# Performance work log

Hardware: AMD Instinct MI355X
Metric: run time of the kernel (lower is better)

Reference implementation:

```python
import jax, jax.numpy as jnp
import numpy as np
import math

B, S, H, NH = 2, 2048, 2048, 16
HD = H // NH
BASE = 10000.0


def _rope_tables():
    inv_freq = 1.0 / (BASE ** (np.arange(0, HD, 2, dtype=np.float32) / HD))
    t = np.arange(S, dtype=np.float32)
    freqs = np.einsum('i,j->ij', t, inv_freq)          # [S, HD/2]
    emb = np.concatenate([freqs, freqs], axis=-1)       # [S, HD]
    return jnp.asarray(np.cos(emb)), jnp.asarray(np.sin(emb))


def setup_inputs() -> dict:
    key = jax.random.key(0)
    ks = jax.random.split(key, 6)
    scale = 1.0 / math.sqrt(H)
    cos, sin = _rope_tables()
    causal = np.triu(np.full((S, S), -1e9, dtype=np.float32), k=1)
    attn_bias = jnp.broadcast_to(jnp.asarray(causal)[None, None], (B, 1, S, S))
    return {
        'hidden_states': jax.random.normal(ks[0], (B, S, H), jnp.float32),
        'masks': jnp.zeros((B, S, S), jnp.float32),
        'attn_bias': attn_bias,
        'cos': cos,
        'sin': sin,
        'wq': jax.random.normal(ks[1], (H, H), jnp.float32) * scale,
        'wk': jax.random.normal(ks[2], (H, H), jnp.float32) * scale,
        'wv': jax.random.normal(ks[3], (H, H), jnp.float32) * scale,
        'wo': jax.random.normal(ks[4], (H, H), jnp.float32) * scale,
        'position_ids': jnp.broadcast_to(jnp.arange(S, dtype=jnp.int64)[None], (B, S)),
    }


def _rotate_half(x):
    x1, x2 = x[..., : x.shape[-1] // 2], x[..., x.shape[-1] // 2:]
    return jnp.concatenate([-x2, x1], axis=-1)


def reference(hidden_states, masks, attn_bias, cos, sin, wq, wk, wv, wo, position_ids):
    b, s, h = hidden_states.shape
    nh, hd = NH, HD
    # QKV projections (torch Linear: x @ W.T), split heads -> [b, nh, s, hd]
    def proj(w):
        return (hidden_states @ w.T).reshape(b, s, nh, hd).transpose(0, 2, 1, 3)
    q, k, v = proj(wq), proj(wk), proj(wv)
    # RoPE
    cos_p = cos[position_ids][:, None]  # [b, 1, s, hd]
    sin_p = sin[position_ids][:, None]
    q = q * cos_p + _rotate_half(q) * sin_p
    k = k * cos_p + _rotate_half(k) * sin_p
    # attention scores with additive masks (mx_attn branch, fp math)
    att = jnp.einsum('bhqd,bhkd->bhqk', q / math.sqrt(hd), k)
    att = att + attn_bias + masks[:, None]
    att = jax.nn.softmax(att, axis=-1)
    out = jnp.einsum('bhqk,bhkd->bhqd', att, v)
    out = out.transpose(0, 2, 1, 3).reshape(b, s, h)
    return out @ wo.T
```

## Files before the change

### kernel.cpp

```cpp
#include <hip/hip_runtime.h>
#include <stdint.h>

#define B_  2
#define S_  2048
#define H_  2048
#define NH_ 16
#define HD_ 128

typedef __bf16 v8bf __attribute__((ext_vector_type(8)));
typedef float  v4f  __attribute__((ext_vector_type(4)));

__device__ __forceinline__ float b2f(unsigned short u) {
  union { unsigned int i; float f; } x; x.i = ((unsigned int)u) << 16; return x.f;
}
__device__ __forceinline__ unsigned short f2b(float f) {
  union { float f; unsigned int i; } x; x.f = f;
  unsigned int r = x.i + 0x7FFFu + ((x.i >> 16) & 1u);
  return (unsigned short)(r >> 16);
}

__device__ __forceinline__ void async16(const void* g, void* l) {
  __builtin_amdgcn_global_load_lds(
      (const __attribute__((address_space(1))) void*)g,
      (__attribute__((address_space(3))) void*)l, 16, 0, 0);
}

__global__ __launch_bounds__(256) void cvt_all(const float* __restrict__ hid,
                                               const float* __restrict__ wq,
                                               const float* __restrict__ wk,
                                               const float* __restrict__ wv,
                                               const float* __restrict__ wo,
                                               unsigned short* __restrict__ Xb,
                                               unsigned short* __restrict__ Wqb,
                                               unsigned short* __restrict__ Wkb,
                                               unsigned short* __restrict__ Wvb,
                                               unsigned short* __restrict__ Wob) {
  int bid = blockIdx.x;
  const float* src;
  unsigned short* dst;
  int rel;
  if (bid < 8192)       { src = hid; dst = Xb;  rel = bid; }
  else if (bid < 12288) { src = wq;  dst = Wqb; rel = bid - 8192; }
  else if (bid < 16384) { src = wk;  dst = Wkb; rel = bid - 12288; }
  else if (bid < 20480) { src = wv;  dst = Wvb; rel = bid - 16384; }
  else                  { src = wo;  dst = Wob; rel = bid - 20480; }
  int i = rel * 256 + threadIdx.x;
  float4 f = *(const float4*)(src + (size_t)i * 4);
  ushort4 u;
  u.x = f2b(f.x); u.y = f2b(f.y); u.z = f2b(f.z); u.w = f2b(f.w);
  *(ushort4*)(dst + (size_t)i * 4) = u;
}

__device__ __forceinline__ void gemm_tile_nt(const unsigned short* __restrict__ A,
                                             const unsigned short* __restrict__ Bm,
                                             int m0, int n0, int Kdim,
                                             unsigned short* As, unsigned short* Bs,
                                             v4f (&acc)[2][8]) {
  const int tid = threadIdx.x;
  const int lane = tid & 63, w = tid >> 6;
  const int lr = lane & 15, lg = lane >> 4;
  const int wm = w * 32;

  for (int k0 = 0; k0 < Kdim; k0 += 32) {
    __syncthreads();
#pragma unroll
    for (int i = 0; i < 2; ++i) {
      const int cbase = i * 256 + w * 64;
      const int cc = cbase + lane;
      const int row = cc >> 2, col = (cc & 3) << 3;
      async16(A  + (size_t)(m0 + row) * Kdim + k0 + col, (char*)As + (size_t)cbase * 16);
      async16(Bm + (size_t)(n0 + row) * Kdim + k0 + col, (char*)Bs + (size_t)cbase * 16);
    }
    __syncthreads();
    v8bf a[2], bb[8];
#pragma unroll
    for (int i = 0; i < 2; i++) a[i]  = *(const v8bf*)(As + (wm + i * 16 + lr) * 32 + lg * 8);
#pragma unroll
    for (int i = 0; i < 8; i++) bb[i] = *(const v8bf*)(Bs + (i * 16 + lr) * 32 + lg * 8);
#pragma unroll
    for (int mi = 0; mi < 2; mi++)
#pragma unroll
      for (int ni = 0; ni < 8; ni++)
        acc[mi][ni] = __builtin_amdgcn_mfma_f32_16x16x32_bf16(a[mi], bb[ni], acc[mi][ni], 0, 0, 0);
  }
}

__global__ __launch_bounds__(512, 2) void gemm_qkv(const unsigned short* __restrict__ X,
                                                   const unsigned short* __restrict__ Wq,
                                                   const unsigned short* __restrict__ Wk,
                                                   const unsigned short* __restrict__ Wv,
                                                   const float* __restrict__ cosT,
                                                   const float* __restrict__ sinT,
                                                   unsigned short* __restrict__ Qo,
                                                   unsigned short* __restrict__ Ko,
                                                   unsigned short* __restrict__ Vt) {
  __shared__ __align__(16) unsigned short lds[4][256 * 64];

  const int tid = threadIdx.x, lane = tid & 63, w = tid >> 6;
  const int lr = lane & 15, lg = lane >> 4;
  const int wm = w >> 1, wn = w & 1;
  const int m0 = blockIdx.x * 256;
  const int ny = blockIdx.y;
  const int sel = ny >> 3;
  const int nt = ny & 7;
  const int n0 = nt * 256;
  const unsigned short* Bw = (sel == 0) ? Wq : (sel == 1 ? Wk : Wv);
  const int xsw = (lr & 7) << 3;

  auto stg = [&](const unsigned short* G, int g0, int k0, unsigned short* dst) {
#pragma unroll
    for (int i = 0; i < 4; ++i) {
      const int cbase = i * 512 + w * 64;
      const int cc = cbase + lane;
      const int row = cc >> 3;
      const int kq = (cc & 7) ^ (row & 7);
      async16(G + (size_t)(g0 + row) * H_ + k0 + kq * 8, (char*)dst + (size_t)cbase * 16);
    }
  };

  v4f acc[4][8];
#pragma unroll
  for (int i = 0; i < 4; i++)
#pragma unroll
    for (int j = 0; j < 8; j++) { v4f z = {0.f, 0.f, 0.f, 0.f}; acc[i][j] = z; }

  stg(X,  m0, 0, lds[0]);
  stg(Bw, n0, 0, lds[1]);
  __syncthreads();

  for (int t = 0; t < 32; ++t) {
    const unsigned short* As = lds[(t & 1) * 2];
    const unsigned short* Bs = lds[(t & 1) * 2 + 1];
    unsigned short* Ad = lds[((t + 1) & 1) * 2];
    unsigned short* Bd = lds[((t + 1) & 1) * 2 + 1];
    const int kn = (t + 1) * 64;
    v8bf bf[8][2], af[2];

    if (t < 31) stg(X, m0, kn, Ad);
#pragma unroll
    for (int ni = 0; ni < 8; ni++) {
      const unsigned short* rp = Bs + (size_t)(wn * 128 + ni * 16 + lr) * 64;
      bf[ni][0] = *(const v8bf*)(rp + ((lg * 8) ^ xsw));
      bf[ni][1] = *(const v8bf*)(rp + ((32 + lg * 8) ^ xsw));
    }
    {
      const unsigned short* rp = As + (size_t)(wm * 64 + lr) * 64;
      af[0] = *(const v8bf*)(rp + ((lg * 8) ^ xsw));
      af[1] = *(const v8bf*)(rp + ((32 + lg * 8) ^ xsw));
    }
    __builtin_amdgcn_s_barrier();
    asm volatile("s_waitcnt lgkmcnt(0)" ::: "memory");
    __builtin_amdgcn_sched_barrier(0);
    __builtin_amdgcn_s_setprio(1);
#pragma unroll
    for (int ni = 0; ni < 8; ni++) {
      acc[0][ni] = __builtin_amdgcn_mfma_f32_16x16x32_bf16(af[0], bf[ni][0], acc[0][ni], 0, 0, 0);
      acc[0][ni] = __builtin_amdgcn_mfma_f32_16x16x32_bf16(af[1], bf[ni][1], acc[0][ni], 0, 0, 0);
    }
    __builtin_amdgcn_s_setprio(0);
    __builtin_amdgcn_s_barrier();

    if (t < 31) stg(Bw, n0, kn, Bd);
    {
      const unsigned short* rp = As + (size_t)(wm * 64 + 16 + lr) * 64;
      af[0] = *(const v8bf*)(rp + ((lg * 8) ^ xsw));
      af[1] = *(const v8bf*)(rp + ((32 + lg * 8) ^ xsw));
    }
    __builtin_amdgcn_s_barrier();
    asm volatile("s_waitcnt lgkmcnt(0)" ::: "memory");
    __builtin_amdgcn_sched_barrier(0);
    __builtin_amdgcn_s_setprio(1);
#pragma unroll
    for (int ni = 0; ni < 8; ni++) {
      acc[1][ni] = __builtin_amdgcn_mfma_f32_16x16x32_bf16(af[0], bf[ni][0], acc[1][ni], 0, 0, 0);
      acc[1][ni] = __builtin_amdgcn_mfma_f32_16x16x32_bf16(af[1], bf[ni][1], acc[1][ni], 0, 0, 0);
    }
    __builtin_amdgcn_s_setprio(0);
    __builtin_amdgcn_s_barrier();

    {
      const unsigned short* rp = As + (size_t)(wm * 64 + 32 + lr) * 64;
      af[0] = *(const v8bf*)(rp + ((lg * 8) ^ xsw));
      af[1] = *(const v8bf*)(rp + ((32 + lg * 8) ^ xsw));
    }
    __builtin_amdgcn_s_barrier();
    asm volatile("s_waitcnt lgkmcnt(0)" ::: "memory");
    __builtin_amdgcn_sched_barrier(0);
    __builtin_amdgcn_s_setprio(1);
#pragma unroll
    for (int ni = 0; ni < 8; ni++) {
      acc[2][ni] = __builtin_amdgcn_mfma_f32_16x16x32_bf16(af[0], bf[ni][0], acc[2][ni], 0, 0, 0);
      acc[2][ni] = __builtin_amdgcn_mfma_f32_16x16x32_bf16(af[1], bf[ni][1], acc[2][ni], 0, 0, 0);
    }
    __builtin_amdgcn_s_setprio(0);
    __builtin_amdgcn_s_barrier();

    {
      const unsigned short* rp = As + (size_t)(wm * 64 + 48 + lr) * 64;
      af[0] = *(const v8bf*)(rp + ((lg * 8) ^ xsw));
      af[1] = *(const v8bf*)(rp + ((32 + lg * 8) ^ xsw));
    }
    __builtin_amdgcn_s_barrier();
    asm volatile("s_waitcnt lgkmcnt(0)" ::: "memory");
    __builtin_amdgcn_sched_barrier(0);
    __builtin_amdgcn_s_setprio(1);
#pragma unroll
    for (int ni = 0; ni < 8; ni++) {
      acc[3][ni] = __builtin_amdgcn_mfma_f32_16x16x32_bf16(af[0], bf[ni][0], acc[3][ni], 0, 0, 0);
      acc[3][ni] = __builtin_amdgcn_mfma_f32_16x16x32_bf16(af[1], bf[ni][1], acc[3][ni], 0, 0, 0);
    }
    __builtin_amdgcn_s_setprio(0);
    __syncthreads();
  }

  const int h = nt * 2 + wn;
  const int rb0 = m0 + wm * 64;
  if (sel < 2) {
    unsigned short* Out = (sel == 0) ? Qo : Ko;
    const float sc = (sel == 0) ? (float)(0.08838834764831845 * 1.4426950408889634) : 1.0f;
#pragma unroll
    for (int mi = 0; mi < 4; mi++)
#pragma unroll
      for (int ni = 0; ni < 4; ni++)
#pragma unroll
        for (int r = 0; r < 4; r++) {
          int row = rb0 + mi * 16 + lg * 4 + r;
          int s = row & 2047;
          int d = ni * 16 + lr;
          float c  = cosT[(size_t)s * HD_ + d];
          float sn = sinT[(size_t)s * HD_ + d];
          float x1 = acc[mi][ni][r], x2 = acc[mi][ni + 4][r];
          Out[(size_t)row * H_ + h * HD_ + d]      = f2b((x1 * c - x2 * sn) * sc);
          Out[(size_t)row * H_ + h * HD_ + d + 64] = f2b((x2 * c + x1 * sn) * sc);
        }
  } else {
#pragma unroll
    for (int mi = 0; mi < 4; mi++)
#pragma unroll
      for (int ni = 0; ni < 8; ni++) {
        int row0 = rb0 + mi * 16 + lg * 4;
        int b = row0 >> 11, s0 = row0 & 2047;
        int d = ni * 16 + lr;
        ushort4 u;
        u.x = f2b(acc[mi][ni][0]); u.y = f2b(acc[mi][ni][1]);
        u.z = f2b(acc[mi][ni][2]); u.w = f2b(acc[mi][ni][3]);
        *(ushort4*)(Vt + ((size_t)((b * NH_ + h) * HD_) + d) * S_ + s0) = u;
      }
  }
}

__global__ __launch_bounds__(256, 2) void gemm_out(const unsigned short* __restrict__ A,
                                                   const unsigned short* __restrict__ Wo,
                                                   float* __restrict__ Out) {
  __shared__ unsigned short As[128 * 32], Bs[128 * 32];
  const int m0 = blockIdx.x * 128;
  const int n0 = blockIdx.y * 128;

  v4f acc[2][8];
#pragma unroll
  for (int i = 0; i < 2; i++)
#pragma unroll
    for (int j = 0; j < 8; j++) { v4f z = {0.f, 0.f, 0.f, 0.f}; acc[i][j] = z; }

  gemm_tile_nt(A, Wo, m0, n0, H_, As, Bs, acc);

  const int lane = threadIdx.x & 63, w = threadIdx.x >> 6;
  const int lr = lane & 15, lg = lane >> 4;
#pragma unroll
  for (int mi = 0; mi < 2; mi++)
#pragma unroll
    for (int ni = 0; ni < 8; ni++)
#pragma unroll
      for (int r = 0; r < 4; r++)
        Out[(size_t)(m0 + w * 32 + mi * 16 + lg * 4 + r) * H_ + n0 + ni * 16 + lr] =
            acc[mi][ni][r];
}

#define KT_ 64

__global__ __launch_bounds__(512, 2) void attn_kernel(const unsigned short* __restrict__ Qb,
                                                      const unsigned short* __restrict__ Kb,
                                                      const unsigned short* __restrict__ Vt,
                                                      unsigned short* __restrict__ Ob) {
  __shared__ __align__(16) char smem[90112];
  unsigned short* Ps = (unsigned short*)(smem + 71680);

  const int tid = threadIdx.x, lane = tid & 63, w = tid >> 6;
  const int lr = lane & 15, lg = lane >> 4;
  const int qp = blockIdx.x, h = blockIdx.y, b = blockIdx.z;

  const int wtile = (w < 4) ? qp : (15 - qp);
  const int wrow = wtile * 128 + (w & 3) * 32;
  const int nkt = (16 - qp) * 2;

  auto stage = [&](int kt, char* Kd) {
    const int k0 = kt * KT_;
    char* Vd = Kd + 17408;
#pragma unroll
    for (int i = 0; i < 3; ++i) {
      int cbase = i * 512 + w * 64;
      if (cbase < 1088) {
        int cc = cbase + lane;
        int row = cc / 17, pos = cc % 17;
        int p2 = (pos == 16) ? 0 : pos;
        async16(Kb + (size_t)(b * S_ + k0 + row) * H_ + h * HD_ + p2 * 8,
                Kd + (size_t)cbase * 16);
      }
    }
#pragma unroll
    for (int i = 0; i < 3; ++i) {
      int cbase = i * 512 + w * 64;
      if (cbase < 1152) {
        int cc = cbase + lane;
        int row = cc / 9, pos = cc % 9;
        int p2 = (pos == 8) ? 0 : pos;
        async16(Vt + ((size_t)((b * NH_ + h) * HD_ + row)) * S_ + k0 + p2 * 8,
                Vd + (size_t)cbase * 16);
      }
    }
  };

  v8bf qf[2][4];
#pragma unroll
  for (int mt = 0; mt < 2; mt++)
#pragma unroll
    for (int ks = 0; ks < 4; ks++)
      qf[mt][ks] = *(const v8bf*)(Qb + (size_t)(b * S_ + wrow + mt * 16 + lr) * H_ +
                                  h * HD_ + ks * 32 + lg * 8);

  v4f o[2][8];
#pragma unroll
  for (int mt = 0; mt < 2; mt++)
#pragma unroll
    for (int nt = 0; nt < 8; nt++) { v4f z = {0.f, 0.f, 0.f, 0.f}; o[mt][nt] = z; }
  float mst[2][4], lst[2][4];
#pragma unroll
  for (int mt = 0; mt < 2; mt++)
#pragma unroll
    for (int r = 0; r < 4; r++) { mst[mt][r] = -1e30f; lst[mt][r] = 0.f; }

  stage(0, smem);
  __syncthreads();

  int cur = 0;
  for (int kt = 0; kt < nkt; kt++) {
    char* curb = smem + cur * 35840;
    if (kt + 1 < nkt) stage(kt + 1, smem + (cur ^ 1) * 35840);

    unsigned short* Ks = (unsigned short*)curb;
    unsigned short* Vs = (unsigned short*)(curb + 17408);
    const int k0 = kt * KT_;

    if (k0 <= wrow + 31) {
      v4f sacc[2][4];
#pragma unroll
      for (int mt = 0; mt < 2; mt++)
#pragma unroll
        for (int nt = 0; nt < 4; nt++) { v4f z = {0.f, 0.f, 0.f, 0.f}; sacc[mt][nt] = z; }
#pragma unroll
      for (int nt = 0; nt < 4; nt++) {
        v8bf kf[4];
#pragma unroll
        for (int ks = 0; ks < 4; ks++)
          kf[ks] = *(const v8bf*)(Ks + (nt * 16 + lr) * 136 + ks * 32 + lg * 8);
#pragma unroll
        for (int mt = 0; mt < 2; mt++)
#pragma unroll
          for (int ks = 0; ks < 4; ks++)
            sacc[mt][nt] =
                __builtin_amdgcn_mfma_f32_16x16x32_bf16(qf[mt][ks], kf[ks], sacc[mt][nt], 0, 0, 0);
      }
      if (k0 + KT_ - 1 > wrow) {
#pragma unroll
        for (int mt = 0; mt < 2; mt++)
#pragma unroll
          for (int nt = 0; nt < 4; nt++)
#pragma unroll
            for (int r = 0; r < 4; r++) {
              int key = k0 + nt * 16 + lr;
              int query = wrow + mt * 16 + lg * 4 + r;
              if (key > query) sacc[mt][nt][r] = -1e30f;
            }
      }
#pragma unroll
      for (int mt = 0; mt < 2; mt++) {
        float rmax[4], alpha[4], rsum[4];
#pragma unroll
        for (int r = 0; r < 4; r++) {
          float v = fmaxf(fmaxf(sacc[mt][0][r], sacc[mt][1][r]),
                          fmaxf(sacc[mt][2][r], sacc[mt][3][r]));
#pragma unroll
          for (int off = 8; off >= 1; off >>= 1) v = fmaxf(v, __shfl_xor(v, off, 64));
          rmax[r] = v;
        }
#pragma unroll
        for (int r = 0; r < 4; r++) {
          float mnew = fmaxf(mst[mt][r], rmax[r]);
          alpha[r] = exp2f(mst[mt][r] - mnew);
          mst[mt][r] = mnew;
          rsum[r] = 0.f;
        }
#pragma unroll
        for (int nt = 0; nt < 4; nt++)
#pragma unroll
          for (int r = 0; r < 4; r++) {
            float p = exp2f(sacc[mt][nt][r] - mst[mt][r]);
            sacc[mt][nt][r] = p;
            rsum[r] += p;
          }
#pragma unroll
        for (int r = 0; r < 4; r++) {
#pragma unroll
          for (int off = 8; off >= 1; off >>= 1) rsum[r] += __shfl_xor(rsum[r], off, 64);
          lst[mt][r] = lst[mt][r] * alpha[r] + rsum[r];
        }
#pragma unroll
        for (int nt = 0; nt < 8; nt++)
#pragma unroll
          for (int r = 0; r < 4; r++) o[mt][nt][r] *= alpha[r];
      }
      v8bf bv[8][2];
#pragma unroll
      for (int nt = 0; nt < 8; nt++)
#pragma unroll
        for (int ks = 0; ks < 2; ks++)
          bv[nt][ks] = *(const v8bf*)(Vs + (nt * 16 + lr) * 72 + ks * 32 + lg * 8);
#pragma unroll
      for (int mt = 0; mt < 2; mt++) {
#pragma unroll
        for (int nt = 0; nt < 4; nt++)
#pragma unroll
          for (int r = 0; r < 4; r++) {
            union { float f; unsigned u; } pu; pu.f = sacc[mt][nt][r];
            Ps[w * 1152 + (lg * 4 + r) * 72 + nt * 16 + lr] =
                (unsigned short)(pu.u >> 16);
          }
        asm volatile("" ::: "memory");
        v8bf af[2];
#pragma unroll
        for (int ks = 0; ks < 2; ks++)
          af[ks] = *(const v8bf*)(Ps + w * 1152 + lr * 72 + ks * 32 + lg * 8);
#pragma unroll
        for (int nt = 0; nt < 8; nt++)
#pragma unroll
          for (int ks = 0; ks < 2; ks++)
            o[mt][nt] = __builtin_amdgcn_mfma_f32_16x16x32_bf16(af[ks], bv[nt][ks], o[mt][nt], 0, 0, 0);
        asm volatile("" ::: "memory");
      }
    }
    __syncthreads();
    cur ^= 1;
  }
#pragma unroll
  for (int mt = 0; mt < 2; mt++) {
    float inv[4];
#pragma unroll
    for (int r = 0; r < 4; r++) inv[r] = 1.f / lst[mt][r];
#pragma unroll
    for (int nt = 0; nt < 8; nt++)
#pragma unroll
      for (int r = 0; r < 4; r++) {
        int row = wrow + mt * 16 + lg * 4 + r;
        int col = h * HD_ + nt * 16 + lr;
        Ob[(size_t)(b * S_ + row) * H_ + col] = f2b(o[mt][nt][r] * inv[r]);
      }
  }
}

extern "C" void kernel_launch(void* const* d_in, const int* in_sizes, int n_in,
                              void* d_out, int out_size, void* d_ws, size_t ws_size,
                              hipStream_t stream) {
  const float* hidden = (const float*)d_in[0];
  const float* cosT = (const float*)d_in[3];
  const float* sinT = (const float*)d_in[4];
  const float* wq = (const float*)d_in[5];
  const float* wk = (const float*)d_in[6];
  const float* wv = (const float*)d_in[7];
  const float* wo = (const float*)d_in[8];
  float* out = (float*)d_out;

  char* p = (char*)d_ws;
  const size_t SZ_X = (size_t)4096 * 2048 * 2;
  const size_t SZ_W = (size_t)2048 * 2048 * 2;
  unsigned short* Xb  = (unsigned short*)p; p += SZ_X;
  unsigned short* Wqb = (unsigned short*)p; p += SZ_W;
  unsigned short* Wkb = (unsigned short*)p; p += SZ_W;
  unsigned short* Wvb = (unsigned short*)p; p += SZ_W;
  unsigned short* Wob = (unsigned short*)p; p += SZ_W;
  unsigned short* Qb  = (unsigned short*)p; p += SZ_X;
  unsigned short* Kb  = (unsigned short*)p; p += SZ_X;
  unsigned short* Vt  = (unsigned short*)p; p += SZ_X;
  unsigned short* Ob  = (unsigned short*)p; p += SZ_X;

  cvt_all<<<24576, 256, 0, stream>>>(hidden, wq, wk, wv, wo, Xb, Wqb, Wkb, Wvb, Wob);
  gemm_qkv<<<dim3(16, 24), 512, 0, stream>>>(Xb, Wqb, Wkb, Wvb, cosT, sinT, Qb, Kb, Vt);
  attn_kernel<<<dim3(8, 16, 2), 512, 0, stream>>>(Qb, Kb, Vt, Ob);
  gemm_out<<<dim3(32, 16), 256, 0, stream>>>(Ob, Wob, out);
}
```

Baseline: 457.2 us.

## Rebalance QKV GEMM work so each block does a Q/K tile plus a V tile

The QKV projection grid goes from 16x24 to 16x16 blocks. Each block now computes one 256x256 Q or K tile with RoPE, then a 256x128 V tile written transposed. Every block gets equal work and the grid is 256 blocks, matching the CU count, which should avoid a ragged tail wave. The cost is more sequential work per block, less parallelism, and a half-width B tile in the V phase that reuses data less well.

```diff
diff --git a/kernel.cpp b/kernel.cpp
--- a/kernel.cpp
+++ b/kernel.cpp
@@ -98,16 +98,11 @@
 
   const int tid = threadIdx.x, lane = tid & 63, w = tid >> 6;
   const int lr = lane & 15, lg = lane >> 4;
-  const int wm = w >> 1, wn = w & 1;
   const int m0 = blockIdx.x * 256;
-  const int ny = blockIdx.y;
-  const int sel = ny >> 3;
-  const int nt = ny & 7;
-  const int n0 = nt * 256;
-  const unsigned short* Bw = (sel == 0) ? Wq : (sel == 1 ? Wk : Wv);
+  const int by = blockIdx.y;
   const int xsw = (lr & 7) << 3;
 
-  auto stg = [&](const unsigned short* G, int g0, int k0, unsigned short* dst) {
+  auto stgA = [&](const unsigned short* G, int g0, int k0, unsigned short* dst) {
 #pragma unroll
     for (int i = 0; i < 4; ++i) {
       const int cbase = i * 512 + w * 64;
@@ -117,107 +112,122 @@
       async16(G + (size_t)(g0 + row) * H_ + k0 + kq * 8, (char*)dst + (size_t)cbase * 16);
     }
   };
-
-  v4f acc[4][8];
-#pragma unroll
-  for (int i = 0; i < 4; i++)
-#pragma unroll
-    for (int j = 0; j < 8; j++) { v4f z = {0.f, 0.f, 0.f, 0.f}; acc[i][j] = z; }
-
-  stg(X,  m0, 0, lds[0]);
-  stg(Bw, n0, 0, lds[1]);
-  __syncthreads();
-
-  for (int t = 0; t < 32; ++t) {
-    const unsigned short* As = lds[(t & 1) * 2];
-    const unsigned short* Bs = lds[(t & 1) * 2 + 1];
-    unsigned short* Ad = lds[((t + 1) & 1) * 2];
-    unsigned short* Bd = lds[((t + 1) & 1) * 2 + 1];
-    const int kn = (t + 1) * 64;
-    v8bf bf[8][2], af[2];
-
-    if (t < 31) stg(X, m0, kn, Ad);
-#pragma unroll
-    for (int ni = 0; ni < 8; ni++) {
-      const unsigned short* rp = Bs + (size_t)(wn * 128 + ni * 16 + lr) * 64;
-      bf[ni][0] = *(const v8bf*)(rp + ((lg * 8) ^ xsw));
-      bf[ni][1] = *(const v8bf*)(rp + ((32 + lg * 8) ^ xsw));
-    }
-    {
-      const unsigned short* rp = As + (size_t)(wm * 64 + lr) * 64;
-      af[0] = *(const v8bf*)(rp + ((lg * 8) ^ xsw));
-      af[1] = *(const v8bf*)(rp + ((32 + lg * 8) ^ xsw));
-    }
-    __builtin_amdgcn_s_barrier();
-    asm volatile("s_waitcnt lgkmcnt(0)" ::: "memory");
-    __builtin_amdgcn_sched_barrier(0);
-    __builtin_amdgcn_s_setprio(1);
-#pragma unroll
-    for (int ni = 0; ni < 8; ni++) {
-      acc[0][ni] = __builtin_amdgcn_mfma_f32_16x16x32_bf16(af[0], bf[ni][0], acc[0][ni], 0, 0, 0);
-      acc[0][ni] = __builtin_amdgcn_mfma_f32_16x16x32_bf16(af[1], bf[ni][1], acc[0][ni], 0, 0, 0);
-    }
-    __builtin_amdgcn_s_setprio(0);
-    __builtin_amdgcn_s_barrier();
-
-    if (t < 31) stg(Bw, n0, kn, Bd);
-    {
-      const unsigned short* rp = As + (size_t)(wm * 64 + 16 + lr) * 64;
-      af[0] = *(const v8bf*)(rp + ((lg * 8) ^ xsw));
-      af[1] = *(const v8bf*)(rp + ((32 + lg * 8) ^ xsw));
-    }
-    __builtin_amdgcn_s_barrier();
-    asm volatile("s_waitcnt lgkmcnt(0)" ::: "memory");
-    __builtin_amdgcn_sched_barrier(0);
-    __builtin_amdgcn_s_setprio(1);
-#pragma unroll
-    for (int ni = 0; ni < 8; ni++) {
-      acc[1][ni] = __builtin_amdgcn_mfma_f32_16x16x32_bf16(af[0], bf[ni][0], acc[1][ni], 0, 0, 0);
-      acc[1][ni] = __builtin_amdgcn_mfma_f32_16x16x32_bf16(af[1], bf[ni][1], acc[1][ni], 0, 0, 0);
-    }
-    __builtin_amdgcn_s_setprio(0);
-    __builtin_amdgcn_s_barrier();
-
-    {
-      const unsigned short* rp = As + (size_t)(wm * 64 + 32 + lr) * 64;
-      af[0] = *(const v8bf*)(rp + ((lg * 8) ^ xsw));
-      af[1] = *(const v8bf*)(rp + ((32 + lg * 8) ^ xsw));
-    }
-    __builtin_amdgcn_s_barrier();
-    asm volatile("s_waitcnt lgkmcnt(0)" ::: "memory");
-    __builtin_amdgcn_sched_barrier(0);
-    __builtin_amdgcn_s_setprio(1);
-#pragma unroll
-    for (int ni = 0; ni < 8; ni++) {
-      acc[2][ni] = __builtin_amdgcn_mfma_f32_16x16x32_bf16(af[0], bf[ni][0], acc[2][ni], 0, 0, 0);
-      acc[2][ni] = __builtin_amdgcn_mfma_f32_16x16x32_bf16(af[1], bf[ni][1], acc[2][ni], 0, 0, 0);
-    }
-    __builtin_amdgcn_s_setprio(0);
-    __builtin_amdgcn_s_barrier();
-
-    {
-      const unsigned short* rp = As + (size_t)(wm * 64 + 48 + lr) * 64;
-      af[0] = *(const v8bf*)(rp + ((lg * 8) ^ xsw));
-      af[1] = *(const v8bf*)(rp + ((32 + lg * 8) ^ xsw));
-    }
-    __builtin_amdgcn_s_barrier();
-    asm volatile("s_waitcnt lgkmcnt(0)" ::: "memory");
-    __builtin_amdgcn_sched_barrier(0);
-    __builtin_amdgcn_s_setprio(1);
-#pragma unroll
-    for (int ni = 0; ni < 8; ni++) {
-      acc[3][ni] = __builtin_amdgcn_mfma_f32_16x16x32_bf16(af[0], bf[ni][0], acc[3][ni], 0, 0, 0);
-      acc[3][ni] = __builtin_amdgcn_mfma_f32_16x16x32_bf16(af[1], bf[ni][1], acc[3][ni], 0, 0, 0);
-    }
-    __builtin_amdgcn_s_setprio(0);
+  auto stgB128 = [&](const unsigned short* G, int g0, int k0, unsigned short* dst) {
+#pragma unroll
+    for (int i = 0; i < 2; ++i) {
+      const int cbase = i * 512 + w * 64;
+      const int cc = cbase + lane;
+      const int row = cc >> 3;
+      const int kq = (cc & 7) ^ (row & 7);
+      async16(G + (size_t)(g0 + row) * H_ + k0 + kq * 8, (char*)dst + (size_t)cbase * 16);
+    }
+  };
+
+  {
+    const int nq = by & 7;
+    const int n0 = nq * 256;
+    const unsigned short* Bw = (by < 8) ? Wq : Wk;
+    const int wm = w >> 1, wn = w & 1;
+
+    v4f acc[4][8];
+#pragma unroll
+    for (int i = 0; i < 4; i++)
+#pragma unroll
+      for (int j = 0; j < 8; j++) { v4f z = {0.f, 0.f, 0.f, 0.f}; acc[i][j] = z; }
+
+    stgA(X,  m0, 0, lds[0]);
+    stgA(Bw, n0, 0, lds[1]);
     __syncthreads();
-  }
-
-  const int h = nt * 2 + wn;
-  const int rb0 = m0 + wm * 64;
-  if (sel < 2) {
-    unsigned short* Out = (sel == 0) ? Qo : Ko;
-    const float sc = (sel == 0) ? (float)(0.08838834764831845 * 1.4426950408889634) : 1.0f;
+
+    for (int t = 0; t < 32; ++t) {
+      const unsigned short* As = lds[(t & 1) * 2];
+      const unsigned short* Bs = lds[(t & 1) * 2 + 1];
+      unsigned short* Ad = lds[((t + 1) & 1) * 2];
+      unsigned short* Bd = lds[((t + 1) & 1) * 2 + 1];
+      const int kn = (t + 1) * 64;
+      v8bf bf[8][2], af[2];
+
+      if (t < 31) stgA(X, m0, kn, Ad);
+#pragma unroll
+      for (int ni = 0; ni < 8; ni++) {
+        const unsigned short* rp = Bs + (size_t)(wn * 128 + ni * 16 + lr) * 64;
+        bf[ni][0] = *(const v8bf*)(rp + ((lg * 8) ^ xsw));
+        bf[ni][1] = *(const v8bf*)(rp + ((32 + lg * 8) ^ xsw));
+      }
+      {
+        const unsigned short* rp = As + (size_t)(wm * 64 + lr) * 64;
+        af[0] = *(const v8bf*)(rp + ((lg * 8) ^ xsw));
+        af[1] = *(const v8bf*)(rp + ((32 + lg * 8) ^ xsw));
+      }
+      __builtin_amdgcn_s_barrier();
+      asm volatile("s_waitcnt lgkmcnt(0)" ::: "memory");
+      __builtin_amdgcn_sched_barrier(0);
+      __builtin_amdgcn_s_setprio(1);
+#pragma unroll
+      for (int ni = 0; ni < 8; ni++) {
+        acc[0][ni] = __builtin_amdgcn_mfma_f32_16x16x32_bf16(af[0], bf[ni][0], acc[0][ni], 0, 0, 0);
+        acc[0][ni] = __builtin_amdgcn_mfma_f32_16x16x32_bf16(af[1], bf[ni][1], acc[0][ni], 0, 0, 0);
+      }
+      __builtin_amdgcn_s_setprio(0);
+      __builtin_amdgcn_s_barrier();
+
+      if (t < 31) stgA(Bw, n0, kn, Bd);
+      {
+        const unsigned short* rp = As + (size_t)(wm * 64 + 16 + lr) * 64;
+        af[0] = *(const v8bf*)(rp + ((lg * 8) ^ xsw));
+        af[1] = *(const v8bf*)(rp + ((32 + lg * 8) ^ xsw));
+      }
+      __builtin_amdgcn_s_barrier();
+      asm volatile("s_waitcnt lgkmcnt(0)" ::: "memory");
+      __builtin_amdgcn_sched_barrier(0);
+      __builtin_amdgcn_s_setprio(1);
+#pragma unroll
+      for (int ni = 0; ni < 8; ni++) {
+        acc[1][ni] = __builtin_amdgcn_mfma_f32_16x16x32_bf16(af[0], bf[ni][0], acc[1][ni], 0, 0, 0);
+        acc[1][ni] = __builtin_amdgcn_mfma_f32_16x16x32_bf16(af[1], bf[ni][1], acc[1][ni], 0, 0, 0);
+      }
+      __builtin_amdgcn_s_setprio(0);
+      __builtin_amdgcn_s_barrier();
+
+      {
+        const unsigned short* rp = As + (size_t)(wm * 64 + 32 + lr) * 64;
+        af[0] = *(const v8bf*)(rp + ((lg * 8) ^ xsw));
+        af[1] = *(const v8bf*)(rp + ((32 + lg * 8) ^ xsw));
+      }
+      __builtin_amdgcn_s_barrier();
+      asm volatile("s_waitcnt lgkmcnt(0)" ::: "memory");
+      __builtin_amdgcn_sched_barrier(0);
+      __builtin_amdgcn_s_setprio(1);
+#pragma unroll
+      for (int ni = 0; ni < 8; ni++) {
+        acc[2][ni] = __builtin_amdgcn_mfma_f32_16x16x32_bf16(af[0], bf[ni][0], acc[2][ni], 0, 0, 0);
+        acc[2][ni] = __builtin_amdgcn_mfma_f32_16x16x32_bf16(af[1], bf[ni][1], acc[2][ni], 0, 0, 0);
+      }
+      __builtin_amdgcn_s_setprio(0);
+      __builtin_amdgcn_s_barrier();
+
+      {
+        const unsigned short* rp = As + (size_t)(wm * 64 + 48 + lr) * 64;
+        af[0] = *(const v8bf*)(rp + ((lg * 8) ^ xsw));
+        af[1] = *(const v8bf*)(rp + ((32 + lg * 8) ^ xsw));
+      }
+      __builtin_amdgcn_s_barrier();
+      asm volatile("s_waitcnt lgkmcnt(0)" ::: "memory");
+      __builtin_amdgcn_sched_barrier(0);
+      __builtin_amdgcn_s_setprio(1);
+#pragma unroll
+      for (int ni = 0; ni < 8; ni++) {
+        acc[3][ni] = __builtin_amdgcn_mfma_f32_16x16x32_bf16(af[0], bf[ni][0], acc[3][ni], 0, 0, 0);
+        acc[3][ni] = __builtin_amdgcn_mfma_f32_16x16x32_bf16(af[1], bf[ni][1], acc[3][ni], 0, 0, 0);
+      }
+      __builtin_amdgcn_s_setprio(0);
+      __syncthreads();
+    }
+
+    const int h = nq * 2 + wn;
+    const int rb0 = m0 + wm * 64;
+    unsigned short* Out = (by < 8) ? Qo : Ko;
+    const float sc = (by < 8) ? (float)(0.08838834764831845 * 1.4426950408889634) : 1.0f;
 #pragma unroll
     for (int mi = 0; mi < 4; mi++)
 #pragma unroll
@@ -233,14 +243,115 @@
           Out[(size_t)row * H_ + h * HD_ + d]      = f2b((x1 * c - x2 * sn) * sc);
           Out[(size_t)row * H_ + h * HD_ + d + 64] = f2b((x2 * c + x1 * sn) * sc);
         }
-  } else {
+  }
+
+  {
+    const int n0v = by * 128;
+    const int wm = w >> 1, wn = w & 1;
+
+    v4f acc[4][4];
+#pragma unroll
+    for (int i = 0; i < 4; i++)
+#pragma unroll
+      for (int j = 0; j < 4; j++) { v4f z = {0.f, 0.f, 0.f, 0.f}; acc[i][j] = z; }
+
+    stgA(X, m0, 0, lds[0]);
+    stgB128(Wv, n0v, 0, lds[1]);
+    __syncthreads();
+
+    for (int t = 0; t < 32; ++t) {
+      const unsigned short* As = lds[(t & 1) * 2];
+      const unsigned short* Bs = lds[(t & 1) * 2 + 1];
+      unsigned short* Ad = lds[((t + 1) & 1) * 2];
+      unsigned short* Bd = lds[((t + 1) & 1) * 2 + 1];
+      const int kn = (t + 1) * 64;
+      v8bf bf[4][2], af[2];
+
+      if (t < 31) stgA(X, m0, kn, Ad);
+#pragma unroll
+      for (int ni = 0; ni < 4; ni++) {
+        const unsigned short* rp = Bs + (size_t)(wn * 64 + ni * 16 + lr) * 64;
+        bf[ni][0] = *(const v8bf*)(rp + ((lg * 8) ^ xsw));
+        bf[ni][1] = *(const v8bf*)(rp + ((32 + lg * 8) ^ xsw));
+      }
+      {
+        const unsigned short* rp = As + (size_t)(wm * 64 + lr) * 64;
+        af[0] = *(const v8bf*)(rp + ((lg * 8) ^ xsw));
+        af[1] = *(const v8bf*)(rp + ((32 + lg * 8) ^ xsw));
+      }
+      __builtin_amdgcn_s_barrier();
+      asm volatile("s_waitcnt lgkmcnt(0)" ::: "memory");
+      __builtin_amdgcn_sched_barrier(0);
+      __builtin_amdgcn_s_setprio(1);
+#pragma unroll
+      for (int ni = 0; ni < 4; ni++) {
+        acc[0][ni] = __builtin_amdgcn_mfma_f32_16x16x32_bf16(af[0], bf[ni][0], acc[0][ni], 0, 0, 0);
+        acc[0][ni] = __builtin_amdgcn_mfma_f32_16x16x32_bf16(af[1], bf[ni][1], acc[0][ni], 0, 0, 0);
+      }
+      __builtin_amdgcn_s_setprio(0);
+      __builtin_amdgcn_s_barrier();
+
+      if (t < 31) stgB128(Wv, n0v, kn, Bd);
+      {
+        const unsigned short* rp = As + (size_t)(wm * 64 + 16 + lr) * 64;
+        af[0] = *(const v8bf*)(rp + ((lg * 8) ^ xsw));
+        af[1] = *(const v8bf*)(rp + ((32 + lg * 8) ^ xsw));
+      }
+      __builtin_amdgcn_s_barrier();
+      asm volatile("s_waitcnt lgkmcnt(0)" ::: "memory");
+      __builtin_amdgcn_sched_barrier(0);
+      __builtin_amdgcn_s_setprio(1);
+#pragma unroll
+      for (int ni = 0; ni < 4; ni++) {
+        acc[1][ni] = __builtin_amdgcn_mfma_f32_16x16x32_bf16(af[0], bf[ni][0], acc[1][ni], 0, 0, 0);
+        acc[1][ni] = __builtin_amdgcn_mfma_f32_16x16x32_bf16(af[1], bf[ni][1], acc[1][ni], 0, 0, 0);
+      }
+      __builtin_amdgcn_s_setprio(0);
+      __builtin_amdgcn_s_barrier();
+
+      {
+        const unsigned short* rp = As + (size_t)(wm * 64 + 32 + lr) * 64;
+        af[0] = *(const v8bf*)(rp + ((lg * 8) ^ xsw));
+        af[1] = *(const v8bf*)(rp + ((32 + lg * 8) ^ xsw));
+      }
+      __builtin_amdgcn_s_barrier();
+      asm volatile("s_waitcnt lgkmcnt(0)" ::: "memory");
+      __builtin_amdgcn_sched_barrier(0);
+      __builtin_amdgcn_s_setprio(1);
+#pragma unroll
+      for (int ni = 0; ni < 4; ni++) {
+        acc[2][ni] = __builtin_amdgcn_mfma_f32_16x16x32_bf16(af[0], bf[ni][0], acc[2][ni], 0, 0, 0);
+        acc[2][ni] = __builtin_amdgcn_mfma_f32_16x16x32_bf16(af[1], bf[ni][1], acc[2][ni], 0, 0, 0);
+      }
+      __builtin_amdgcn_s_setprio(0);
+      __builtin_amdgcn_s_barrier();
+
+      {
+        const unsigned short* rp = As + (size_t)(wm * 64 + 48 + lr) * 64;
+        af[0] = *(const v8bf*)(rp + ((lg * 8) ^ xsw));
+        af[1] = *(const v8bf*)(rp + ((32 + lg * 8) ^ xsw));
+      }
+      __builtin_amdgcn_s_barrier();
+      asm volatile("s_waitcnt lgkmcnt(0)" ::: "memory");
+      __builtin_amdgcn_sched_barrier(0);
+      __builtin_amdgcn_s_setprio(1);
+#pragma unroll
+      for (int ni = 0; ni < 4; ni++) {
+        acc[3][ni] = __builtin_amdgcn_mfma_f32_16x16x32_bf16(af[0], bf[ni][0], acc[3][ni], 0, 0, 0);
+        acc[3][ni] = __builtin_amdgcn_mfma_f32_16x16x32_bf16(af[1], bf[ni][1], acc[3][ni], 0, 0, 0);
+      }
+      __builtin_amdgcn_s_setprio(0);
+      __syncthreads();
+    }
+
+    const int h = by;
 #pragma unroll
     for (int mi = 0; mi < 4; mi++)
 #pragma unroll
-      for (int ni = 0; ni < 8; ni++) {
-        int row0 = rb0 + mi * 16 + lg * 4;
+      for (int ni = 0; ni < 4; ni++) {
+        int row0 = m0 + wm * 64 + mi * 16 + lg * 4;
         int b = row0 >> 11, s0 = row0 & 2047;
-        int d = ni * 16 + lr;
+        int d = wn * 64 + ni * 16 + lr;
         ushort4 u;
         u.x = f2b(acc[mi][ni][0]); u.y = f2b(acc[mi][ni][1]);
         u.z = f2b(acc[mi][ni][2]); u.w = f2b(acc[mi][ni][3]);
@@ -493,7 +604,7 @@
   unsigned short* Ob  = (unsigned short*)p; p += SZ_X;
 
   cvt_all<<<24576, 256, 0, stream>>>(hidden, wq, wk, wv, wo, Xb, Wqb, Wkb, Wvb, Wob);
-  gemm_qkv<<<dim3(16, 24), 512, 0, stream>>>(Xb, Wqb, Wkb, Wvb, cosT, sinT, Qb, Kb, Vt);
+  gemm_qkv<<<dim3(16, 16), 512, 0, stream>>>(Xb, Wqb, Wkb, Wvb, cosT, sinT, Qb, Kb, Vt);
   attn_kernel<<<dim3(8, 16, 2), 512, 0, stream>>>(Qb, Kb, Vt, Ob);
   gemm_out<<<dim3(32, 16), 256, 0, stream>>>(Ob, Wob, out);
 }
```

Result: faster. 434.3 us (-5.0%).
